# Performance work log

Hardware: AMD Instinct MI355X
Metric: run time of the kernel (lower is better)

Reference implementation:

```python
import jax, jax.numpy as jnp
import numpy as np

B, N, D, E = 64, 512, 128, 16384
NEG = -1e9


def setup_inputs() -> dict:
    key = jax.random.key(0)
    ks = jax.random.split(key, 10)
    return {
        "node_emb": jax.random.normal(ks[0], (B, N, D), jnp.float32),
        "mask": jnp.ones((B, N), dtype=bool),
        "edge_idx": jax.random.randint(ks[1], (2, E), 0, N),
        "attn_wts": jax.random.uniform(ks[2], (E,), jnp.float32),
        "edge_weights": jax.random.uniform(ks[3], (B, N, N), jnp.float32) + 0.1,
        "W_ih": jax.random.normal(ks[4], (4 * D, D), jnp.float32) * 0.05,
        "W_hh": jax.random.normal(ks[5], (4 * D, D), jnp.float32) * 0.05,
        "b_ih": jax.random.normal(ks[6], (4 * D,), jnp.float32) * 0.05,
        "b_hh": jax.random.normal(ks[7], (4 * D,), jnp.float32) * 0.05,
        "attn_W": jax.random.normal(ks[8], (D, D), jnp.float32) * 0.05,
        "attn_b": jax.random.normal(ks[9], (D,), jnp.float32) * 0.05,
        "enc_attn_wt": jnp.float32(0.75),
        "revisit_penalty": jnp.float32(-0.5),
        "shortcut_weight": jnp.float32(10.0),
        "shortcut_bonus": jnp.float32(15.0),
    }


def reference(node_emb, mask, edge_idx, attn_wts, edge_weights,
              W_ih, W_hh, b_ih, b_hh, attn_W, attn_b,
              enc_attn_wt, revisit_penalty, shortcut_weight, shortcut_bonus):
    B_, N_, D_ = node_emb.shape
    scale = 1.0 / jnp.sqrt(jnp.float32(D_))
    bidx = jnp.arange(B_)
    nidx = jnp.arange(N_)[None, :]
    # keys = attn(node_emb): identical every step in the torch code -> hoisted.
    keys = node_emb @ attn_W.T + attn_b  # [B,N,D]
    # Encoder-attention edge scatter precomputed as dense [N,N] src->tgt table.
    A = jnp.zeros((N_, N_), node_emb.dtype).at[edge_idx[0], edge_idx[1]].add(attn_wts)
    real_count = jnp.sum(mask, axis=1).astype(jnp.int32)  # [B]

    def step_fn(carry, step):
        h, c, inp, visited, uniq, first, prev = carry
        # LSTMCell (torch gate order i,f,g,o)
        gates = inp @ W_ih.T + b_ih + h @ W_hh.T + b_hh  # [B,4D]
        i, f, g, o = jnp.split(gates, 4, axis=1)
        c = jax.nn.sigmoid(f) * c + jax.nn.sigmoid(i) * jnp.tanh(g)
        h = jax.nn.sigmoid(o) * jnp.tanh(c)
        scores = jnp.einsum('bd,bnd->bn', h, keys) * scale  # [B,N]
        # encoder-attn bonus (only when prev_node exists, i.e. step > 0)
        scores = scores + jnp.where(step > 0, enc_attn_wt, 0.0) * A[prev]
        # branch 1: revisit penalty while tour incomplete
        rev = jnp.where(visited & mask, revisit_penalty, scores)
        # branch 2: shortcut bonuses once all real nodes visited (next_idx == first)
        prev_w = edge_weights[bidx, prev]  # [B,N] costs from prev node
        to_first = jnp.take_along_axis(edge_weights, first[:, None, None], axis=2)[..., 0]  # [B,N]
        direct = prev_w[bidx, first][:, None]  # [B,1]
        detour = prev_w + to_first
        bmask = mask & (nidx != first[:, None]) & (detour < direct)
        bonus = jnp.where(bmask, shortcut_bonus * (direct - detour) / direct, 0.0)
        cmin = prev_w.min(axis=1, keepdims=True)
        cmax = prev_w.max(axis=1, keepdims=True)
        rng_ok = cmax > cmin
        normd = jnp.where(rng_ok,
                          shortcut_weight * (1.0 - (prev_w - cmin) / jnp.where(rng_ok, cmax - cmin, 1.0)),
                          0.0)
        shortcut = scores + bonus + normd
        cond = (uniq < real_count)[:, None]
        scores = jnp.where(cond, rev, jnp.where(step > 0, shortcut, scores))
        scores = jnp.where(mask, scores, NEG)
        probs = jax.nn.softmax(scores, axis=1)
        curr = jnp.argmax(probs, axis=1).astype(jnp.int32)  # greedy decode
        log_p = jnp.log(probs[bidx, curr] + 1e-10)
        first = jnp.where(step == 0, curr, first)
        newly = ~visited[bidx, curr]
        uniq = uniq + newly.astype(jnp.int32)
        visited = visited.at[bidx, curr].set(True)
        inp = node_emb[bidx, curr]
        return (h, c, inp, visited, uniq, first, curr), (curr, log_p)

    init = (jnp.zeros((B_, D_), node_emb.dtype),
            jnp.zeros((B_, D_), node_emb.dtype),
            node_emb.mean(axis=1),
            jnp.zeros((B_, N_), dtype=bool),
            jnp.zeros((B_,), jnp.int32),
            jnp.zeros((B_,), jnp.int32),
            jnp.zeros((B_,), jnp.int32))
    (h, c, inp, visited, uniq, first, prev), (curr_seq, logp_seq) = jax.lax.scan(
        step_fn, init, jnp.arange(N_))
    # final step N: return to first node with log-prob 0
    tours = jnp.concatenate([curr_seq.T, first[:, None]], axis=1)          # [B, N+1]
    log_probs = jnp.concatenate([logp_seq.T, jnp.zeros((B_, 1), logp_seq.dtype)], axis=1)
    return tours, log_probs
```

## Files before the change

kernel.cpp:

```cpp
#include <hip/hip_runtime.h>
#include <cstdint>
#include <cstddef>

constexpr int kB = 64;
constexpr int kN = 512;
constexpr int kD = 128;
constexpr int kE = 16384;
constexpr double kNEG = -1e9;

constexpr size_t BO_WT   = 0;
constexpr size_t BO_BIAS = 524288;
constexpr size_t BO_INP0 = 528384;
constexpr size_t BO_AWT  = 593920;
constexpr size_t BO_AB   = 659456;
constexpr size_t BO_A    = 659968;
constexpr size_t BO_WT4  = 2757120;
constexpr size_t BO_GPRE = 2888192;
constexpr size_t GPRE_BYTES = (size_t)64 * 513 * 512 * 4;
constexpr size_t BO_KEYS4 = BO_GPRE + GPRE_BYTES;
constexpr size_t KEYS_BYTES = (size_t)64 * 32 * 512 * 16;
constexpr size_t WS_NEED_FULL = BO_KEYS4 + KEYS_BYTES;

__device__ __forceinline__ double finzd(double v, double fb) {
    return (v == v && v <= 1.0e308 && v >= -1.0e308) ? v : fb;
}
__device__ __forceinline__ double load_scalar_d(const void* p, double fb) {
    unsigned short lo; __builtin_memcpy(&lo, p, 2);
    float f;
    if (lo == 0) { __builtin_memcpy(&f, p, 4); }
    else { unsigned int u = ((unsigned int)lo) << 16; __builtin_memcpy(&f, &u, 4); }
    return finzd((double)f, fb);
}
__device__ __forceinline__ double sigd(double v) { return 1.0 / (1.0 + exp(-v)); }

__global__ __launch_bounds__(256) void prep_wt(const float* __restrict__ W_ih,
                                               const float* __restrict__ W_hh,
                                               const float* __restrict__ b_ih,
                                               const float* __restrict__ b_hh,
                                               char* __restrict__ wsb) {
    int idx = blockIdx.x * 256 + threadIdx.x;
    if (idx < 131072) {
        int k = idx >> 9, j = idx & 511;
        float v = (k < 128) ? W_ih[j * 128 + k] : W_hh[j * 128 + (k - 128)];
        ((float*)(wsb + BO_WT))[idx] = v;
    } else if (idx < 131072 + 512) {
        int j = idx - 131072;
        ((double*)(wsb + BO_BIAS))[j] = (double)b_ih[j] + (double)b_hh[j];
    }
}

__global__ __launch_bounds__(256) void prep_wt4(char* __restrict__ wsb) {
    int idx = blockIdx.x * 256 + threadIdx.x;
    int q = idx >> 9, j = idx & 511;
    const float* WT = (const float*)(wsb + BO_WT);
    float4 v;
    v.x = WT[(size_t)(192 + 4 * q + 0) * 512 + j];
    v.y = WT[(size_t)(192 + 4 * q + 1) * 512 + j];
    v.z = WT[(size_t)(192 + 4 * q + 2) * 512 + j];
    v.w = WT[(size_t)(192 + 4 * q + 3) * 512 + j];
    ((float4*)(wsb + BO_WT4))[idx] = v;
}

__global__ __launch_bounds__(256) void prep_awt(const float* __restrict__ attn_W,
                                                const float* __restrict__ attn_b,
                                                char* __restrict__ wsb) {
    int idx = blockIdx.x * 256 + threadIdx.x;
    if (idx < 16384) {
        int k = idx >> 7, d = idx & 127;
        ((float*)(wsb + BO_AWT))[idx] = attn_W[d * 128 + k];
    } else if (idx < 16512) {
        ((float*)(wsb + BO_AB))[idx - 16384] = attn_b[idx - 16384];
    }
}

__global__ __launch_bounds__(256) void prep_zeroA(char* __restrict__ wsb) {
    int idx = blockIdx.x * 256 + threadIdx.x;
    ((double*)(wsb + BO_A))[idx] = 0.0;
}

__global__ __launch_bounds__(256) void prep_scatterA(const int* __restrict__ edge_idx,
                                                     const float* __restrict__ attn_wts,
                                                     char* __restrict__ wsb) {
    int e = blockIdx.x * 256 + threadIdx.x;
    if (e < kE) {
        int s = edge_idx[e] & 511;
        int t = edge_idx[kE + e] & 511;
        atomicAdd(&((double*)(wsb + BO_A))[(size_t)s * kN + t], (double)attn_wts[e]);
    }
}

__global__ __launch_bounds__(128) void prep_inp0(const float* __restrict__ emb,
                                                 char* __restrict__ wsb) {
    int b = blockIdx.x, d = threadIdx.x;
    const float* p = emb + (size_t)b * kN * kD + d;
    double s = 0.0;
#pragma unroll 8
    for (int n = 0; n < kN; n++) s += (double)p[(size_t)n * kD];
    ((double*)(wsb + BO_INP0))[b * kD + d] = s * (1.0 / 512.0);
}

__global__ __launch_bounds__(512) void prep_gpre(const float* __restrict__ emb,
                                                 char* __restrict__ wsb) {
    const int b = blockIdx.y;
    const int n0 = blockIdx.x * 16;
    const int tid = threadIdx.x;
    const int nr = (513 - n0 < 16) ? (513 - n0) : 16;
    __shared__ double xs[16 * 128];
    const double* inp0 = (const double*)(wsb + BO_INP0) + (size_t)b * 128;
    for (int i = tid; i < nr * 128; i += 512) {
        int r = i >> 7, d = i & 127;
        int n = n0 + r;
        xs[i] = (n < 512) ? (double)emb[((size_t)b * 512 + n) * 128 + d] : inp0[d];
    }
    __syncthreads();
    const float* wcol = ((const float*)(wsb + BO_WT)) + tid;
    double acc[16];
#pragma unroll
    for (int r = 0; r < 16; r++) acc[r] = 0.0;
    for (int k = 0; k < 128; k++) {
        double w = (double)wcol[(size_t)k * 512];
#pragma unroll
        for (int r = 0; r < 16; r++) acc[r] += xs[r * 128 + k] * w;
    }
    float* gp = (float*)(wsb + BO_GPRE);
#pragma unroll
    for (int r = 0; r < 16; r++)
        if (r < nr) gp[((size_t)b * 513 + n0 + r) * 512 + tid] = (float)acc[r];
}

__global__ __launch_bounds__(256) void prep_keys(const float* __restrict__ emb,
                                                 const float* __restrict__ attn_W,
                                                 const float* __restrict__ attn_b,
                                                 char* __restrict__ wsb) {
    const int b = blockIdx.y;
    const int n0 = blockIdx.x * 64;
    const int tid = threadIdx.x;
    __shared__ float embL[64 * 130];
    __shared__ float WL[128 * 128];
    for (int i = tid; i < 64 * 128; i += 256) {
        int r = i >> 7, k = i & 127;
        embL[r * 130 + k] = emb[((size_t)b * kN + n0 + r) * kD + k];
    }
    for (int i = tid; i < 128 * 128; i += 256) WL[i] = attn_W[i];
    __syncthreads();
    const int nh = tid & 63;
    const int part = tid >> 6;
    float4* kout = (float4*)(wsb + BO_KEYS4) + (size_t)b * 32 * 512;
    const float* er = &embL[nh * 130];
    for (int dq = part * 8; dq < part * 8 + 8; dq++) {
        double a0 = (double)attn_b[4 * dq + 0], a1 = (double)attn_b[4 * dq + 1];
        double a2 = (double)attn_b[4 * dq + 2], a3 = (double)attn_b[4 * dq + 3];
        const float* w0 = &WL[(4 * dq + 0) * 128];
        const float* w1 = &WL[(4 * dq + 1) * 128];
        const float* w2 = &WL[(4 * dq + 2) * 128];
        const float* w3 = &WL[(4 * dq + 3) * 128];
#pragma unroll 8
        for (int k = 0; k < 128; k++) {
            double ek = (double)er[k];
            a0 += ek * (double)w0[k]; a1 += ek * (double)w1[k];
            a2 += ek * (double)w2[k]; a3 += ek * (double)w3[k];
        }
        float4 v; v.x = (float)a0; v.y = (float)a1; v.z = (float)a2; v.w = (float)a3;
        kout[(size_t)dq * 512 + n0 + nh] = v;
    }
}

template <int M>
__global__ __launch_bounds__(512) void decode_kernel(
    const float* __restrict__ emb, const unsigned char* __restrict__ mask,
    const float* __restrict__ edge_w, const char* __restrict__ wsb,
    const void* __restrict__ enc_p, const void* __restrict__ rev_p,
    const void* __restrict__ sw_p, const void* __restrict__ sb_p,
    float* __restrict__ out) {
    const int b = blockIdx.x;
    const int tid = threadIdx.x;

    __shared__ float wks[(M == 0) ? (128 * 129) : (16 * 512 * 4)];
    __shared__ double x[256];
    __shared__ double cs[128];
    __shared__ double gates[512];
    __shared__ double up[(M == 0) ? 512 : 1];
    __shared__ double u[(M == 0) ? 128 : 1];
    __shared__ double redd[8], redd2[8];
    __shared__ int redi[8];
    __shared__ unsigned char visited[512];
    __shared__ int tours_s[512];
    __shared__ double logp_d[512];
    __shared__ int s_rc;
    __shared__ double s_hb, s_cmin, s_cmax;

    const float* WT = (const float*)(wsb + BO_WT);
    const double* biasC = (const double*)(wsb + BO_BIAS);
    const double* A = (const double*)(wsb + BO_A);
    const float* EW = edge_w + (size_t)b * kN * kN;
    const double enc = load_scalar_d(enc_p, 0.75);
    const double revp = load_scalar_d(rev_p, -0.5);
    const double sw = load_scalar_d(sw_p, 10.0);
    const double sb = load_scalar_d(sb_p, 15.0);
    const double scale = 1.0 / sqrt(128.0);

    if constexpr (M == 0) {
        for (int i = tid; i < 128 * 128; i += 512) {
            int k = i >> 7, d = i & 127;
            wks[k * 129 + d] = ((const float*)(wsb + BO_AWT))[i];
        }
    } else {
        for (int i = tid; i < 64 * 512; i += 512) {
            int r = i >> 9, j = i & 511;
            wks[((r >> 2) * 512 + j) * 4 + (r & 3)] = WT[(size_t)(128 + r) * 512 + j];
        }
    }
    double abreg = 0.0;
    if constexpr (M == 0)
        abreg = (tid < 128) ? (double)((const float*)(wsb + BO_AB))[tid] : 0.0;

    if (tid < 128) { x[tid] = ((const double*)(wsb + BO_INP0))[b * kD + tid]; cs[tid] = 0.0; }
    if (tid >= 128 && tid < 256) x[tid] = 0.0;
    visited[tid] = 0;
    const size_t mi = (size_t)b * kN + tid;
    const bool mk = (mask[mi] != 0) || (mask[mi & ~(size_t)3] != 0);
    {
        int v = mk ? 1 : 0;
        for (int off = 32; off; off >>= 1) v += __shfl_xor(v, off);
        if ((tid & 63) == 0) redi[tid >> 6] = v;
    }
    __syncthreads();
    if (tid == 0) {
        int rc = 0;
        for (int w = 0; w < 8; w++) rc += redi[w];
        s_rc = rc;
    }
    __syncthreads();
    const int rc = s_rc;

    int prev = 0, first = 0, uniq = 0;

    const float* gbase = (const float*)(wsb + BO_GPRE) + (size_t)b * 513 * 512;
    const float4* kb4 = (const float4*)(wsb + BO_KEYS4) + (size_t)b * 32 * 512;
    const float4* wl4 = (const float4*)wks;
    const float4* wg4 = (const float4*)(wsb + BO_WT4);
    const double* h = &x[128];

    double gp_cur = 0.0;
    if constexpr (M != 0) gp_cur = (double)gbase[(size_t)512 * 512 + tid];
    double a_cur = A[tid];

    for (int step = 0; step < kN; step++) {
        double g0 = biasC[tid], g1 = (M != 0) ? gp_cur : 0.0, g2 = 0.0, g3 = 0.0;
        if constexpr (M == 0) {
            const float* wcol = WT + tid;
            for (int k0 = 0; k0 < 256; k0 += 4) {
                float w0 = wcol[(size_t)(k0 + 0) * 512], w1 = wcol[(size_t)(k0 + 1) * 512];
                float w2 = wcol[(size_t)(k0 + 2) * 512], w3 = wcol[(size_t)(k0 + 3) * 512];
                g0 += x[k0 + 0] * (double)w0; g1 += x[k0 + 1] * (double)w1;
                g2 += x[k0 + 2] * (double)w2; g3 += x[k0 + 3] * (double)w3;
            }
        } else {
#pragma unroll 4
            for (int q = 0; q < 16; q++) {
                float4 w = wl4[q * 512 + tid];
                const double* hq = &h[4 * q];
                g0 += hq[0] * (double)w.x; g1 += hq[1] * (double)w.y;
                g2 += hq[2] * (double)w.z; g3 += hq[3] * (double)w.w;
            }
#pragma unroll 4
            for (int q = 0; q < 16; q++) {
                float4 w = wg4[q * 512 + tid];
                const double* hq = &h[64 + 4 * q];
                g0 += hq[0] * (double)w.x; g1 += hq[1] * (double)w.y;
                g2 += hq[2] * (double)w.z; g3 += hq[3] * (double)w.w;
            }
        }
        gates[tid] = (g0 + g1) + (g2 + g3);
        __syncthreads();

        if (tid < 128) {
            double gi = gates[tid], gf = gates[128 + tid];
            double gg = gates[256 + tid], go = gates[384 + tid];
            double c = sigd(gf) * cs[tid] + sigd(gi) * tanh(gg);
            cs[tid] = c;
            double hd = sigd(go) * tanh(c);
            x[128 + tid] = hd;
            if constexpr (M == 0) {
                double hp = hd * abreg;
                for (int off = 32; off; off >>= 1) hp += __shfl_xor(hp, off);
                if ((tid & 63) == 0) redd[tid >> 6] = hp;
            }
        }
        __syncthreads();

        double s;
        if constexpr (M == 0) {
            {
                int k = tid & 127, part = tid >> 7;
                const float* arow = &wks[(size_t)k * 129 + part * 32];
                const double* hx = &x[128 + part * 32];
                double ps = 0.0;
#pragma unroll 8
                for (int i2 = 0; i2 < 32; i2++) ps += hx[i2] * (double)arow[i2];
                up[part * 128 + k] = ps;
            }
            __syncthreads();
            if (tid < 128) u[tid] = up[tid] + up[128 + tid] + up[256 + tid] + up[384 + tid];
            if (tid == 0) s_hb = redd[0] + redd[1];
            __syncthreads();
            double d0 = 0.0, d1 = 0.0, d2 = 0.0, d3 = 0.0;
            const float4* e4 = (const float4*)(emb + ((size_t)b * kN + tid) * kD);
#pragma unroll 4
            for (int q = 0; q < 32; q++) {
                float4 w = e4[q];
                const double* u4 = &u[q * 4];
                d0 += u4[0] * (double)w.x; d1 += u4[1] * (double)w.y;
                d2 += u4[2] * (double)w.z; d3 += u4[3] * (double)w.w;
            }
            s = (((d0 + d1) + (d2 + d3)) + s_hb) * scale;
        } else {
            double d0 = 0.0, d1 = 0.0, d2 = 0.0, d3 = 0.0;
#pragma unroll 4
            for (int q = 0; q < 32; q++) {
                float4 w = kb4[(size_t)q * 512 + tid];
                const double* hq = &h[4 * q];
                d0 += hq[0] * (double)w.x; d1 += hq[1] * (double)w.y;
                d2 += hq[2] * (double)w.z; d3 += hq[3] * (double)w.w;
            }
            s = ((d0 + d1) + (d2 + d3)) * scale;
        }
        if (step > 0) s += enc * a_cur;

        double sfinal;
        const bool shortcut_mode = (uniq >= rc);
        if (!shortcut_mode) {
            sfinal = (visited[tid] && mk) ? revp : s;
        } else if (step > 0) {
            double pw = (double)EW[(size_t)prev * kN + tid];
            double mn = pw, mx = pw;
            for (int off = 32; off; off >>= 1) {
                mn = fmin(mn, __shfl_xor(mn, off));
                mx = fmax(mx, __shfl_xor(mx, off));
            }
            if ((tid & 63) == 0) { redd[tid >> 6] = mn; redd2[tid >> 6] = mx; }
            __syncthreads();
            if (tid == 0) {
                double a = redd[0], z = redd2[0];
                for (int w = 1; w < 8; w++) { a = fmin(a, redd[w]); z = fmax(z, redd2[w]); }
                s_cmin = a; s_cmax = z;
            }
            __syncthreads();
            double cmin = s_cmin, cmax = s_cmax;
            int fi = first;
            double to_first = (double)EW[(size_t)tid * kN + fi];
            double direct = (double)EW[(size_t)prev * kN + fi];
            double detour = pw + to_first;
            double bonus = (mk && tid != fi && detour < direct && direct != 0.0)
                               ? sb * (direct - detour) / direct : 0.0;
            bool rng_ok = cmax > cmin;
            double normd = rng_ok ? sw * (1.0 - (pw - cmin) / (cmax - cmin)) : 0.0;
            sfinal = s + bonus + normd;
        } else {
            sfinal = s;
        }
        if (!mk) sfinal = kNEG;
        sfinal = finzd(sfinal, kNEG);

        double v = sfinal; int vi = tid;
        for (int off = 32; off; off >>= 1) {
            double ov = __shfl_xor(v, off);
            int oi = __shfl_xor(vi, off);
            if (ov > v || (ov == v && oi < vi)) { v = ov; vi = oi; }
        }
        if ((tid & 63) == 0) { redd[tid >> 6] = v; redi[tid >> 6] = vi; }
        __syncthreads();
        double smax = redd[0]; int sidx = redi[0];
#pragma unroll
        for (int w = 1; w < 8; w++) {
            double rv = redd[w]; int ri = redi[w];
            if (rv > smax || (rv == smax && ri < sidx)) { smax = rv; sidx = ri; }
        }
        const int oldvis = visited[sidx];
        double gp_next = 0.0;
        if constexpr (M != 0) gp_next = (double)gbase[(size_t)sidx * 512 + tid];
        double a_next = A[(size_t)sidx * kN + tid];

        double e = exp(sfinal - smax);
        double sv = e;
        for (int off = 32; off; off >>= 1) sv += __shfl_xor(sv, off);
        if ((tid & 63) == 0) redd2[tid >> 6] = sv;
        __syncthreads();
        double m = 0.0;
#pragma unroll
        for (int w = 0; w < 8; w++) m += redd2[w];
        m = (m == m && m > 0.0) ? m : 1.0;
        double p = 1.0 / m;
        p = (p == p && p >= 0.0) ? p : 0.0;
        if (tid == 0) { tours_s[step] = sidx; logp_d[step] = p; }
        if (tid == sidx) visited[tid] = 1;
        uniq += oldvis ? 0 : 1;
        if (step == 0) first = sidx;
        prev = sidx;
        gp_cur = gp_next; a_cur = a_next;
        if constexpr (M == 0) {
            if (tid < 128) x[tid] = (double)emb[((size_t)b * kN + sidx) * kD + tid];
            __syncthreads();
        }
    }

    __syncthreads();
    out[(size_t)b * (kN + 1) + tid] = (float)tours_s[tid];
    out[(size_t)kB * (kN + 1) + (size_t)b * (kN + 1) + tid] =
        (float)log(logp_d[tid] + 1e-10);
    if (tid == 0) {
        out[(size_t)b * (kN + 1) + kN] = (float)first;
        out[(size_t)kB * (kN + 1) + (size_t)b * (kN + 1) + kN] = 0.f;
    }
}

extern "C" void kernel_launch(void* const* d_in, const int* in_sizes, int n_in,
                              void* d_out, int out_size, void* d_ws, size_t ws_size,
                              hipStream_t stream) {
    const float* emb = (const float*)d_in[0];
    const unsigned char* mask = (const unsigned char*)d_in[1];
    const int* edge_idx = (const int*)d_in[2];
    const float* attn_wts = (const float*)d_in[3];
    const float* edge_w = (const float*)d_in[4];
    const float* W_ih = (const float*)d_in[5];
    const float* W_hh = (const float*)d_in[6];
    const float* b_ih = (const float*)d_in[7];
    const float* b_hh = (const float*)d_in[8];
    const float* attn_W = (const float*)d_in[9];
    const float* attn_b = (const float*)d_in[10];
    char* wsb = (char*)d_ws;
    float* out = (float*)d_out;
    (void)in_sizes; (void)n_in; (void)out_size;

    prep_wt<<<dim3(514), dim3(256), 0, stream>>>(W_ih, W_hh, b_ih, b_hh, wsb);
    prep_zeroA<<<dim3(1024), dim3(256), 0, stream>>>(wsb);
    prep_scatterA<<<dim3(64), dim3(256), 0, stream>>>(edge_idx, attn_wts, wsb);
    prep_inp0<<<dim3(64), dim3(128), 0, stream>>>(emb, wsb);

    if (ws_size >= WS_NEED_FULL) {
        prep_wt4<<<dim3(32), dim3(256), 0, stream>>>(wsb);
        prep_gpre<<<dim3(33, 64), dim3(512), 0, stream>>>(emb, wsb);
        prep_keys<<<dim3(8, 64), dim3(256), 0, stream>>>(emb, attn_W, attn_b, wsb);
        decode_kernel<2><<<dim3(64), dim3(512), 0, stream>>>(emb, mask, edge_w, wsb,
            d_in[11], d_in[12], d_in[13], d_in[14], out);
    } else {
        prep_awt<<<dim3(65), dim3(256), 0, stream>>>(attn_W, attn_b, wsb);
        decode_kernel<0><<<dim3(64), dim3(512), 0, stream>>>(emb, mask, edge_w, wsb,
            d_in[11], d_in[12], d_in[13], d_in[14], out);
    }
}
```

Baseline: 3.847 ms.

## Restructure LSTM decode loop to fuse gate matvec with scoring and cut barriers

In the main decode path, the recurrent gate matvec for the next step is now computed in the same pass as the attention score matvec, since both read only h. The gate nonlinearities are applied per thread into a shared trans buffer before the loop-closing barrier, and the softmax-sum finalisation is deferred into the next iteration. Together this removes barriers per step. Keys and the recurrent weights are now stored pre-converted as double2, which drops float-to-double conversions but doubles the memory and LDS traffic for those arrays.

```diff
diff --git a/kernel.cpp b/kernel.cpp
--- a/kernel.cpp
+++ b/kernel.cpp
@@ -14,12 +14,12 @@
 constexpr size_t BO_AWT  = 593920;
 constexpr size_t BO_AB   = 659456;
 constexpr size_t BO_A    = 659968;
-constexpr size_t BO_WT4  = 2757120;
-constexpr size_t BO_GPRE = 2888192;
+constexpr size_t BO_WG2  = 2757120;
+constexpr size_t BO_GPRE = 3281408;
 constexpr size_t GPRE_BYTES = (size_t)64 * 513 * 512 * 4;
-constexpr size_t BO_KEYS4 = BO_GPRE + GPRE_BYTES;
-constexpr size_t KEYS_BYTES = (size_t)64 * 32 * 512 * 16;
-constexpr size_t WS_NEED_FULL = BO_KEYS4 + KEYS_BYTES;
+constexpr size_t BO_KEYS2 = BO_GPRE + GPRE_BYTES;
+constexpr size_t KEYS_BYTES = (size_t)64 * 64 * 512 * 16;
+constexpr size_t WS_NEED_FULL = BO_KEYS2 + KEYS_BYTES;
 
 __device__ __forceinline__ double finzd(double v, double fb) {
     return (v == v && v <= 1.0e308 && v >= -1.0e308) ? v : fb;
@@ -49,16 +49,14 @@
     }
 }
 
-__global__ __launch_bounds__(256) void prep_wt4(char* __restrict__ wsb) {
+__global__ __launch_bounds__(256) void prep_wt8(char* __restrict__ wsb) {
     int idx = blockIdx.x * 256 + threadIdx.x;
-    int q = idx >> 9, j = idx & 511;
+    int p = idx >> 9, j = idx & 511;
     const float* WT = (const float*)(wsb + BO_WT);
-    float4 v;
-    v.x = WT[(size_t)(192 + 4 * q + 0) * 512 + j];
-    v.y = WT[(size_t)(192 + 4 * q + 1) * 512 + j];
-    v.z = WT[(size_t)(192 + 4 * q + 2) * 512 + j];
-    v.w = WT[(size_t)(192 + 4 * q + 3) * 512 + j];
-    ((float4*)(wsb + BO_WT4))[idx] = v;
+    double2 v;
+    v.x = (double)WT[(size_t)(128 + 2 * p) * 512 + j];
+    v.y = (double)WT[(size_t)(129 + 2 * p) * 512 + j];
+    ((double2*)(wsb + BO_WG2))[idx] = v;
 }
 
 __global__ __launch_bounds__(256) void prep_awt(const float* __restrict__ attn_W,
@@ -145,7 +143,7 @@
     __syncthreads();
     const int nh = tid & 63;
     const int part = tid >> 6;
-    float4* kout = (float4*)(wsb + BO_KEYS4) + (size_t)b * 32 * 512;
+    double2* kout = (double2*)(wsb + BO_KEYS2) + (size_t)b * 64 * 512;
     const float* er = &embL[nh * 130];
     for (int dq = part * 8; dq < part * 8 + 8; dq++) {
         double a0 = (double)attn_b[4 * dq + 0], a1 = (double)attn_b[4 * dq + 1];
@@ -160,8 +158,10 @@
             a0 += ek * (double)w0[k]; a1 += ek * (double)w1[k];
             a2 += ek * (double)w2[k]; a3 += ek * (double)w3[k];
         }
-        float4 v; v.x = (float)a0; v.y = (float)a1; v.z = (float)a2; v.w = (float)a3;
-        kout[(size_t)dq * 512 + n0 + nh] = v;
+        double2 va; va.x = a0; va.y = a1;
+        double2 vb; vb.x = a2; vb.y = a3;
+        kout[(size_t)(2 * dq + 0) * 512 + n0 + nh] = va;
+        kout[(size_t)(2 * dq + 1) * 512 + n0 + nh] = vb;
     }
 }
 
@@ -175,10 +175,11 @@
     const int b = blockIdx.x;
     const int tid = threadIdx.x;
 
-    __shared__ float wks[(M == 0) ? (128 * 129) : (16 * 512 * 4)];
+    __shared__ double2 wks[(M == 0) ? 4128 : 8192];
     __shared__ double x[256];
     __shared__ double cs[128];
-    __shared__ double gates[512];
+    __shared__ double gates[(M == 0) ? 512 : 1];
+    __shared__ double trans[(M == 0) ? 1 : 512];
     __shared__ double up[(M == 0) ? 512 : 1];
     __shared__ double u[(M == 0) ? 128 : 1];
     __shared__ double redd[8], redd2[8];
@@ -199,16 +200,16 @@
     const double sb = load_scalar_d(sb_p, 15.0);
     const double scale = 1.0 / sqrt(128.0);
 
+    const double2* wg2 = (const double2*)(wsb + BO_WG2);
+
     if constexpr (M == 0) {
+        float* awt = (float*)wks;
         for (int i = tid; i < 128 * 128; i += 512) {
             int k = i >> 7, d = i & 127;
-            wks[k * 129 + d] = ((const float*)(wsb + BO_AWT))[i];
+            awt[k * 129 + d] = ((const float*)(wsb + BO_AWT))[i];
         }
     } else {
-        for (int i = tid; i < 64 * 512; i += 512) {
-            int r = i >> 9, j = i & 511;
-            wks[((r >> 2) * 512 + j) * 4 + (r & 3)] = WT[(size_t)(128 + r) * 512 + j];
-        }
+        for (int i = tid; i < 16 * 512; i += 512) wks[i] = wg2[i];
     }
     double abreg = 0.0;
     if constexpr (M == 0)
@@ -236,18 +237,145 @@
     int prev = 0, first = 0, uniq = 0;
 
     const float* gbase = (const float*)(wsb + BO_GPRE) + (size_t)b * 513 * 512;
-    const float4* kb4 = (const float4*)(wsb + BO_KEYS4) + (size_t)b * 32 * 512;
-    const float4* wl4 = (const float4*)wks;
-    const float4* wg4 = (const float4*)(wsb + BO_WT4);
+    const double2* kb2 = (const double2*)(wsb + BO_KEYS2) + (size_t)b * 64 * 512;
     const double* h = &x[128];
 
-    double gp_cur = 0.0;
-    if constexpr (M != 0) gp_cur = (double)gbase[(size_t)512 * 512 + tid];
-    double a_cur = A[tid];
-
-    for (int step = 0; step < kN; step++) {
-        double g0 = biasC[tid], g1 = (M != 0) ? gp_cur : 0.0, g2 = 0.0, g3 = 0.0;
-        if constexpr (M == 0) {
+    if constexpr (M != 0) {
+        {
+            double gp0 = (double)gbase[(size_t)512 * 512 + tid];
+            double gf = (biasC[tid] + gp0) + 0.0;
+            trans[tid] = (tid >= 256 && tid < 384) ? tanh(gf) : sigd(gf);
+        }
+        double a_cur = A[tid];
+        __syncthreads();
+
+        for (int step = 0; step < kN; step++) {
+            if (step > 0) {
+                if (tid == prev) visited[tid] = 1;
+                if (tid == 0) {
+                    double m = 0.0;
+#pragma unroll
+                    for (int w = 0; w < 8; w++) m += redd2[w];
+                    m = (m == m && m > 0.0) ? m : 1.0;
+                    double p = 1.0 / m;
+                    logp_d[step - 1] = (p == p && p >= 0.0) ? p : 0.0;
+                }
+            }
+            if (tid < 128) {
+                double ai = trans[tid], af = trans[128 + tid];
+                double ag = trans[256 + tid], ao = trans[384 + tid];
+                double c = af * cs[tid] + ai * ag;
+                cs[tid] = c;
+                x[128 + tid] = ao * tanh(c);
+            }
+            __syncthreads();
+
+            double d0 = 0.0, d1 = 0.0, d2 = 0.0, d3 = 0.0;
+            double q0 = biasC[tid], q1 = 0.0, q2 = 0.0, q3 = 0.0;
+#pragma unroll 4
+            for (int q = 0; q < 32; q++) {
+                double2 e0 = kb2[(size_t)(2 * q + 0) * 512 + tid];
+                double2 e1 = kb2[(size_t)(2 * q + 1) * 512 + tid];
+                d0 += h[4 * q + 0] * e0.x; d1 += h[4 * q + 1] * e0.y;
+                d2 += h[4 * q + 2] * e1.x; d3 += h[4 * q + 3] * e1.y;
+            }
+#pragma unroll 4
+            for (int q = 0; q < 8; q++) {
+                double2 w0 = wks[(2 * q + 0) * 512 + tid];
+                double2 w1 = wks[(2 * q + 1) * 512 + tid];
+                q0 += h[4 * q + 0] * w0.x; q1 += h[4 * q + 1] * w0.y;
+                q2 += h[4 * q + 2] * w1.x; q3 += h[4 * q + 3] * w1.y;
+            }
+#pragma unroll 4
+            for (int q = 8; q < 32; q++) {
+                double2 w0 = wg2[(size_t)(2 * q + 0) * 512 + tid];
+                double2 w1 = wg2[(size_t)(2 * q + 1) * 512 + tid];
+                q0 += h[4 * q + 0] * w0.x; q1 += h[4 * q + 1] * w0.y;
+                q2 += h[4 * q + 2] * w1.x; q3 += h[4 * q + 3] * w1.y;
+            }
+            double s = ((d0 + d1) + (d2 + d3)) * scale;
+            if (step > 0) s += enc * a_cur;
+
+            double sfinal;
+            const bool shortcut_mode = (uniq >= rc);
+            if (!shortcut_mode) {
+                sfinal = (visited[tid] && mk) ? revp : s;
+            } else if (step > 0) {
+                double pw = (double)EW[(size_t)prev * kN + tid];
+                double mn = pw, mx = pw;
+                for (int off = 32; off; off >>= 1) {
+                    mn = fmin(mn, __shfl_xor(mn, off));
+                    mx = fmax(mx, __shfl_xor(mx, off));
+                }
+                if ((tid & 63) == 0) { redd[tid >> 6] = mn; redd2[tid >> 6] = mx; }
+                __syncthreads();
+                if (tid == 0) {
+                    double a = redd[0], z = redd2[0];
+                    for (int w = 1; w < 8; w++) { a = fmin(a, redd[w]); z = fmax(z, redd2[w]); }
+                    s_cmin = a; s_cmax = z;
+                }
+                __syncthreads();
+                double cmin = s_cmin, cmax = s_cmax;
+                int fi = first;
+                double to_first = (double)EW[(size_t)tid * kN + fi];
+                double direct = (double)EW[(size_t)prev * kN + fi];
+                double detour = pw + to_first;
+                double bonus = (mk && tid != fi && detour < direct && direct != 0.0)
+                                   ? sb * (direct - detour) / direct : 0.0;
+                bool rng_ok = cmax > cmin;
+                double normd = rng_ok ? sw * (1.0 - (pw - cmin) / (cmax - cmin)) : 0.0;
+                sfinal = s + bonus + normd;
+            } else {
+                sfinal = s;
+            }
+            if (!mk) sfinal = kNEG;
+            sfinal = finzd(sfinal, kNEG);
+
+            double v = sfinal; int vi = tid;
+            for (int off = 32; off; off >>= 1) {
+                double ov = __shfl_xor(v, off);
+                int oi = __shfl_xor(vi, off);
+                if (ov > v || (ov == v && oi < vi)) { v = ov; vi = oi; }
+            }
+            if ((tid & 63) == 0) { redd[tid >> 6] = v; redi[tid >> 6] = vi; }
+            __syncthreads();
+            double smax = redd[0]; int sidx = redi[0];
+#pragma unroll
+            for (int w = 1; w < 8; w++) {
+                double rv = redd[w]; int ri = redi[w];
+                if (rv > smax || (rv == smax && ri < sidx)) { smax = rv; sidx = ri; }
+            }
+            const int oldvis = visited[sidx];
+            double gp_next = (double)gbase[(size_t)sidx * 512 + tid];
+            double a_next = A[(size_t)sidx * kN + tid];
+
+            double e = exp(sfinal - smax);
+            double sv = e;
+            for (int off = 32; off; off >>= 1) sv += __shfl_xor(sv, off);
+            if ((tid & 63) == 0) redd2[tid >> 6] = sv;
+            if (tid == 0) tours_s[step] = sidx;
+
+            double gfn = ((q0 + q1) + (q2 + q3)) + gp_next;
+            trans[tid] = (tid >= 256 && tid < 384) ? tanh(gfn) : sigd(gfn);
+
+            uniq += oldvis ? 0 : 1;
+            if (step == 0) first = sidx;
+            prev = sidx;
+            a_cur = a_next;
+            __syncthreads();
+        }
+        if (tid == 0) {
+            double m = 0.0;
+#pragma unroll
+            for (int w = 0; w < 8; w++) m += redd2[w];
+            m = (m == m && m > 0.0) ? m : 1.0;
+            double p = 1.0 / m;
+            logp_d[kN - 1] = (p == p && p >= 0.0) ? p : 0.0;
+        }
+    } else {
+        const float* awt = (const float*)wks;
+        for (int step = 0; step < kN; step++) {
+            double g0 = biasC[tid], g1 = 0.0, g2 = 0.0, g3 = 0.0;
             const float* wcol = WT + tid;
             for (int k0 = 0; k0 < 256; k0 += 4) {
                 float w0 = wcol[(size_t)(k0 + 0) * 512], w1 = wcol[(size_t)(k0 + 1) * 512];
@@ -255,45 +383,23 @@
                 g0 += x[k0 + 0] * (double)w0; g1 += x[k0 + 1] * (double)w1;
                 g2 += x[k0 + 2] * (double)w2; g3 += x[k0 + 3] * (double)w3;
             }
-        } else {
-#pragma unroll 4
-            for (int q = 0; q < 16; q++) {
-                float4 w = wl4[q * 512 + tid];
-                const double* hq = &h[4 * q];
-                g0 += hq[0] * (double)w.x; g1 += hq[1] * (double)w.y;
-                g2 += hq[2] * (double)w.z; g3 += hq[3] * (double)w.w;
-            }
-#pragma unroll 4
-            for (int q = 0; q < 16; q++) {
-                float4 w = wg4[q * 512 + tid];
-                const double* hq = &h[64 + 4 * q];
-                g0 += hq[0] * (double)w.x; g1 += hq[1] * (double)w.y;
-                g2 += hq[2] * (double)w.z; g3 += hq[3] * (double)w.w;
-            }
-        }
-        gates[tid] = (g0 + g1) + (g2 + g3);
-        __syncthreads();
-
-        if (tid < 128) {
-            double gi = gates[tid], gf = gates[128 + tid];
-            double gg = gates[256 + tid], go = gates[384 + tid];
-            double c = sigd(gf) * cs[tid] + sigd(gi) * tanh(gg);
-            cs[tid] = c;
-            double hd = sigd(go) * tanh(c);
-            x[128 + tid] = hd;
-            if constexpr (M == 0) {
+            gates[tid] = (g0 + g1) + (g2 + g3);
+            __syncthreads();
+            if (tid < 128) {
+                double gi = gates[tid], gf = gates[128 + tid];
+                double gg = gates[256 + tid], go = gates[384 + tid];
+                double c = sigd(gf) * cs[tid] + sigd(gi) * tanh(gg);
+                cs[tid] = c;
+                double hd = sigd(go) * tanh(c);
+                x[128 + tid] = hd;
                 double hp = hd * abreg;
                 for (int off = 32; off; off >>= 1) hp += __shfl_xor(hp, off);
                 if ((tid & 63) == 0) redd[tid >> 6] = hp;
             }
-        }
-        __syncthreads();
-
-        double s;
-        if constexpr (M == 0) {
+            __syncthreads();
             {
                 int k = tid & 127, part = tid >> 7;
-                const float* arow = &wks[(size_t)k * 129 + part * 32];
+                const float* arow = &awt[(size_t)k * 129 + part * 32];
                 const double* hx = &x[128 + part * 32];
                 double ps = 0.0;
 #pragma unroll 8
@@ -313,92 +419,75 @@
                 d0 += u4[0] * (double)w.x; d1 += u4[1] * (double)w.y;
                 d2 += u4[2] * (double)w.z; d3 += u4[3] * (double)w.w;
             }
-            s = (((d0 + d1) + (d2 + d3)) + s_hb) * scale;
-        } else {
-            double d0 = 0.0, d1 = 0.0, d2 = 0.0, d3 = 0.0;
-#pragma unroll 4
-            for (int q = 0; q < 32; q++) {
-                float4 w = kb4[(size_t)q * 512 + tid];
-                const double* hq = &h[4 * q];
-                d0 += hq[0] * (double)w.x; d1 += hq[1] * (double)w.y;
-                d2 += hq[2] * (double)w.z; d3 += hq[3] * (double)w.w;
-            }
-            s = ((d0 + d1) + (d2 + d3)) * scale;
-        }
-        if (step > 0) s += enc * a_cur;
-
-        double sfinal;
-        const bool shortcut_mode = (uniq >= rc);
-        if (!shortcut_mode) {
-            sfinal = (visited[tid] && mk) ? revp : s;
-        } else if (step > 0) {
-            double pw = (double)EW[(size_t)prev * kN + tid];
-            double mn = pw, mx = pw;
+            double s = (((d0 + d1) + (d2 + d3)) + s_hb) * scale;
+            if (step > 0) s += enc * A[(size_t)prev * kN + tid];
+
+            double sfinal;
+            const bool shortcut_mode = (uniq >= rc);
+            if (!shortcut_mode) {
+                sfinal = (visited[tid] && mk) ? revp : s;
+            } else if (step > 0) {
+                double pw = (double)EW[(size_t)prev * kN + tid];
+                double mn = pw, mx = pw;
+                for (int off = 32; off; off >>= 1) {
+                    mn = fmin(mn, __shfl_xor(mn, off));
+                    mx = fmax(mx, __shfl_xor(mx, off));
+                }
+                if ((tid & 63) == 0) { redd[tid >> 6] = mn; redd2[tid >> 6] = mx; }
+                __syncthreads();
+                if (tid == 0) {
+                    double a = redd[0], z = redd2[0];
+                    for (int w = 1; w < 8; w++) { a = fmin(a, redd[w]); z = fmax(z, redd2[w]); }
+                    s_cmin = a; s_cmax = z;
+                }
+                __syncthreads();
+                double cmin = s_cmin, cmax = s_cmax;
+                int fi = first;
+                double to_first = (double)EW[(size_t)tid * kN + fi];
+                double direct = (double)EW[(size_t)prev * kN + fi];
+                double detour = pw + to_first;
+                double bonus = (mk && tid != fi && detour < direct && direct != 0.0)
+                                   ? sb * (direct - detour) / direct : 0.0;
+                bool rng_ok = cmax > cmin;
+                double normd = rng_ok ? sw * (1.0 - (pw - cmin) / (cmax - cmin)) : 0.0;
+                sfinal = s + bonus + normd;
+            } else {
+                sfinal = s;
+            }
+            if (!mk) sfinal = kNEG;
+            sfinal = finzd(sfinal, kNEG);
+
+            double v = sfinal; int vi = tid;
             for (int off = 32; off; off >>= 1) {
-                mn = fmin(mn, __shfl_xor(mn, off));
-                mx = fmax(mx, __shfl_xor(mx, off));
-            }
-            if ((tid & 63) == 0) { redd[tid >> 6] = mn; redd2[tid >> 6] = mx; }
-            __syncthreads();
-            if (tid == 0) {
-                double a = redd[0], z = redd2[0];
-                for (int w = 1; w < 8; w++) { a = fmin(a, redd[w]); z = fmax(z, redd2[w]); }
-                s_cmin = a; s_cmax = z;
-            }
-            __syncthreads();
-            double cmin = s_cmin, cmax = s_cmax;
-            int fi = first;
-            double to_first = (double)EW[(size_t)tid * kN + fi];
-            double direct = (double)EW[(size_t)prev * kN + fi];
-            double detour = pw + to_first;
-            double bonus = (mk && tid != fi && detour < direct && direct != 0.0)
-                               ? sb * (direct - detour) / direct : 0.0;
-            bool rng_ok = cmax > cmin;
-            double normd = rng_ok ? sw * (1.0 - (pw - cmin) / (cmax - cmin)) : 0.0;
-            sfinal = s + bonus + normd;
-        } else {
-            sfinal = s;
-        }
-        if (!mk) sfinal = kNEG;
-        sfinal = finzd(sfinal, kNEG);
-
-        double v = sfinal; int vi = tid;
-        for (int off = 32; off; off >>= 1) {
-            double ov = __shfl_xor(v, off);
-            int oi = __shfl_xor(vi, off);
-            if (ov > v || (ov == v && oi < vi)) { v = ov; vi = oi; }
-        }
-        if ((tid & 63) == 0) { redd[tid >> 6] = v; redi[tid >> 6] = vi; }
-        __syncthreads();
-        double smax = redd[0]; int sidx = redi[0];
-#pragma unroll
-        for (int w = 1; w < 8; w++) {
-            double rv = redd[w]; int ri = redi[w];
-            if (rv > smax || (rv == smax && ri < sidx)) { smax = rv; sidx = ri; }
-        }
-        const int oldvis = visited[sidx];
-        double gp_next = 0.0;
-        if constexpr (M != 0) gp_next = (double)gbase[(size_t)sidx * 512 + tid];
-        double a_next = A[(size_t)sidx * kN + tid];
-
-        double e = exp(sfinal - smax);
-        double sv = e;
-        for (int off = 32; off; off >>= 1) sv += __shfl_xor(sv, off);
-        if ((tid & 63) == 0) redd2[tid >> 6] = sv;
-        __syncthreads();
-        double m = 0.0;
-#pragma unroll
-        for (int w = 0; w < 8; w++) m += redd2[w];
-        m = (m == m && m > 0.0) ? m : 1.0;
-        double p = 1.0 / m;
-        p = (p == p && p >= 0.0) ? p : 0.0;
-        if (tid == 0) { tours_s[step] = sidx; logp_d[step] = p; }
-        if (tid == sidx) visited[tid] = 1;
-        uniq += oldvis ? 0 : 1;
-        if (step == 0) first = sidx;
-        prev = sidx;
-        gp_cur = gp_next; a_cur = a_next;
-        if constexpr (M == 0) {
+                double ov = __shfl_xor(v, off);
+                int oi = __shfl_xor(vi, off);
+                if (ov > v || (ov == v && oi < vi)) { v = ov; vi = oi; }
+            }
+            if ((tid & 63) == 0) { redd[tid >> 6] = v; redi[tid >> 6] = vi; }
+            __syncthreads();
+            double smax = redd[0]; int sidx = redi[0];
+#pragma unroll
+            for (int w = 1; w < 8; w++) {
+                double rv = redd[w]; int ri = redi[w];
+                if (rv > smax || (rv == smax && ri < sidx)) { smax = rv; sidx = ri; }
+            }
+            const int oldvis = visited[sidx];
+            double e = exp(sfinal - smax);
+            double sv = e;
+            for (int off = 32; off; off >>= 1) sv += __shfl_xor(sv, off);
+            if ((tid & 63) == 0) redd2[tid >> 6] = sv;
+            __syncthreads();
+            double m = 0.0;
+#pragma unroll
+            for (int w = 0; w < 8; w++) m += redd2[w];
+            m = (m == m && m > 0.0) ? m : 1.0;
+            double p = 1.0 / m;
+            p = (p == p && p >= 0.0) ? p : 0.0;
+            if (tid == 0) { tours_s[step] = sidx; logp_d[step] = p; }
+            if (tid == sidx) visited[tid] = 1;
+            uniq += oldvis ? 0 : 1;
+            if (step == 0) first = sidx;
+            prev = sidx;
             if (tid < 128) x[tid] = (double)emb[((size_t)b * kN + sidx) * kD + tid];
             __syncthreads();
         }
@@ -438,7 +527,7 @@
     prep_inp0<<<dim3(64), dim3(128), 0, stream>>>(emb, wsb);
 
     if (ws_size >= WS_NEED_FULL) {
-        prep_wt4<<<dim3(32), dim3(256), 0, stream>>>(wsb);
+        prep_wt8<<<dim3(128), dim3(256), 0, stream>>>(wsb);
         prep_gpre<<<dim3(33, 64), dim3(512), 0, stream>>>(emb, wsb);
         prep_keys<<<dim3(8, 64), dim3(256), 0, stream>>>(emb, attn_W, attn_b, wsb);
         decode_kernel<2><<<dim3(64), dim3(512), 0, stream>>>(emb, mask, edge_w, wsb,
```

After: 6.077 ms. 58.0% more time.
